# Kernel optimization log

Measured on AMD Instinct MI355X. Metric: run time of the kernel, lower is better.

The kernel has to match this reference:

```python
import jax, jax.numpy as jnp
import numpy as np

N = 50000
E = 800000
IN_C, HID, OUT_C, HEADS = 128, 64, 32, 2
NEG_SLOPE = 0.2


def _add_self_loops(edge_index, n):
    loop = jnp.arange(n, dtype=edge_index.dtype)
    return jnp.concatenate([edge_index, jnp.stack([loop, loop])], axis=1)


def gcn_conv(x, edge_index, W, b, n):
    ei = _add_self_loops(edge_index, n)
    src, dst = ei[0], ei[1]
    h = x @ W                                    # [N, out]
    deg = jax.ops.segment_sum(jnp.ones_like(dst, dtype=h.dtype), dst, num_segments=n)
    dinv = jnp.where(deg > 0, jax.lax.rsqrt(deg), 0.0)
    norm = dinv[src] * dinv[dst]                 # [E2]
    out = jax.ops.segment_sum(h[src] * norm[:, None], dst, num_segments=n)
    return out + b


def gat_conv(x, edge_index, W, att_src, att_dst, b, n, heads, out_dim, concat):
    ei = _add_self_loops(edge_index, n)
    src, dst = ei[0], ei[1]
    h = (x @ W).reshape(n, heads, out_dim)       # [N, H, C]
    a_s = jnp.sum(h * att_src, axis=-1)          # [N, H]
    a_d = jnp.sum(h * att_dst, axis=-1)          # [N, H]
    e = a_s[src] + a_d[dst]                      # [E2, H]
    e = jnp.where(e > 0, e, NEG_SLOPE * e)       # leaky_relu
    # edge softmax grouped by destination node
    m = jax.ops.segment_max(e, dst, num_segments=n)          # [N, H]
    ex = jnp.exp(e - m[dst])
    s = jax.ops.segment_sum(ex, dst, num_segments=n)          # [N, H]
    alpha = ex / s[dst]                          # [E2, H]
    out = jax.ops.segment_sum(h[src] * alpha[:, :, None], dst, num_segments=n)  # [N, H, C]
    if concat:
        out = out.reshape(n, heads * out_dim)
    else:
        out = out.mean(axis=1)
    return out + b


def setup_inputs() -> dict:
    key = jax.random.key(0)
    ks = jax.random.split(key, 16)
    x = jax.random.normal(ks[0], (N, IN_C), dtype=jnp.float32)
    edge_index = jax.random.randint(ks[1], (2, E), 0, N, dtype=jnp.int64)

    def glorot(k, shape):
        fan = shape[0] + shape[-1]
        return jax.random.normal(k, shape, dtype=jnp.float32) * np.sqrt(2.0 / fan)

    return {
        "x": x,
        "edge_index": edge_index,
        "W1": glorot(ks[2], (IN_C, HID)),
        "b1": jnp.zeros((HID,), jnp.float32),
        "W2": glorot(ks[3], (HID, HID)),
        "b2": jnp.zeros((HID,), jnp.float32),
        "Wg1": glorot(ks[4], (HID, HEADS * HID)),
        "as1": glorot(ks[5], (HEADS, HID)),
        "ad1": glorot(ks[6], (HEADS, HID)),
        "bg1": jnp.zeros((HEADS * HID,), jnp.float32),
        "Wg2": glorot(ks[7], (HEADS * HID, HEADS * OUT_C)),
        "as2": glorot(ks[8], (HEADS, OUT_C)),
        "ad2": glorot(ks[9], (HEADS, OUT_C)),
        "bg2": jnp.zeros((OUT_C,), jnp.float32),
    }


def reference(x, edge_index, W1, b1, W2, b2, Wg1, as1, ad1, bg1, Wg2, as2, ad2, bg2):
    n = x.shape[0]
    h = jax.nn.relu(gcn_conv(x, edge_index, W1, b1, n))
    h = jax.nn.relu(gcn_conv(h, edge_index, W2, b2, n))
    h = jax.nn.relu(gat_conv(h, edge_index, Wg1, as1, ad1, bg1, n, HEADS, HID, True))
    h = gat_conv(h, edge_index, Wg2, as2, ad2, bg2, n, HEADS, OUT_C, False)
    return jax.nn.log_softmax(h, axis=1)
```

## Files before the change

kernel.cpp:

```cpp
#include <hip/hip_runtime.h>

#define NN 50000
#define EE 800000
#define NEG 0.2f
#define CAP 64
#define NBC 98
#define BSH2 9
#define CAPB 16384
#define PCH 3125

typedef long long i64;
typedef unsigned int u32;
typedef unsigned short u16;
typedef __attribute__((ext_vector_type(8))) short bf16x8;
typedef __attribute__((ext_vector_type(4))) float f32x4;

static __device__ __forceinline__ u16 f2bf(float f) {
  u32 u = __float_as_uint(f);
  u += 0x7FFFu + ((u >> 16) & 1u);
  return (u16)(u >> 16);
}
static __device__ __forceinline__ float bflo(u32 v) { return __uint_as_float(v << 16); }
static __device__ __forceinline__ float bfhi(u32 v) { return __uint_as_float(v & 0xffff0000u); }
static __device__ __forceinline__ u32 pack2bf(float a, float b) {
  return (u32)f2bf(a) | ((u32)f2bf(b) << 16);
}
static __device__ __forceinline__ void fma8(float* acc, int4 v, float a) {
  acc[0] += bflo(v.x) * a; acc[1] += bfhi(v.x) * a;
  acc[2] += bflo(v.y) * a; acc[3] += bfhi(v.y) * a;
  acc[4] += bflo(v.z) * a; acc[5] += bfhi(v.z) * a;
  acc[6] += bflo(v.w) * a; acc[7] += bfhi(v.w) * a;
}

__global__ void k_probe(const void* ei, int* flag, int* gcnt) {
  __shared__ int sbad[4];
  int t = threadIdx.x;
  if (t < NBC) gcnt[t] = 0;
  const i64* p = (const i64*)ei;
  i64 v = p[t];
  int bad = (v < 0 || v >= NN) ? 1 : 0;
  unsigned long long b = __ballot(bad);
  if ((t & 63) == 0) sbad[t >> 6] = (b != 0ULL);
  __syncthreads();
  if (t == 0) *flag = !(sbad[0] | sbad[1] | sbad[2] | sbad[3]);
}

static __device__ __forceinline__ int edge_at(const void* ei, int is64, int idx) {
  return is64 ? (int)((const i64*)ei)[idx] : ((const int*)ei)[idx];
}

__global__ void k_part(const void* ei, const int* flag, int* gcnt, u32* buf) {
  __shared__ u32 lbuf[PCH];
  __shared__ int hist[128], offb[128], curb[128], gbase[128], sc[128];
  int t = threadIdx.x;
  int is64 = *flag;
  if (t < 128) { hist[t] = 0; curb[t] = 0; }
  __syncthreads();
  int lo = blockIdx.x * PCH;

  for (int e = lo + t; e < lo + PCH; e += 256)
    atomicAdd(&hist[edge_at(ei, is64, EE + e) >> BSH2], 1);
  __syncthreads();

  if (t < 128) sc[t] = hist[t];
  __syncthreads();
  for (int o = 1; o < 128; o <<= 1) {
    int v = (t >= o && t < 128) ? sc[t - o] : 0;
    __syncthreads();
    if (t < 128) sc[t] += v;
    __syncthreads();
  }
  if (t < 128) offb[t] = sc[t] - hist[t];
  __syncthreads();

  for (int e = lo + t; e < lo + PCH; e += 256) {
    int s = edge_at(ei, is64, e);
    int d = edge_at(ei, is64, EE + e);
    int b = d >> BSH2;
    u32 v = (u32)s | ((u32)(d & 511) << 16) | ((u32)b << 25);
    int p = atomicAdd(&curb[b], 1);
    lbuf[offb[b] + p] = v;
  }
  __syncthreads();

  if (t < 128) {
    int c = hist[t];
    gbase[t] = c ? atomicAdd(&gcnt[t], c) : 0;
  }
  __syncthreads();

  for (int i = t; i < PCH; i += 256) {
    u32 v = lbuf[i];
    int b = v >> 25;
    int pos = gbase[b] + (i - offb[b]);
    if (pos < CAPB) buf[(size_t)b * CAPB + pos] = v;
  }
}

__global__ void k_scanb(const int* gcnt, int* csrbase, int* rowp) {
  __shared__ int sc[128];
  int t = threadIdx.x;
  int c = (t < NBC) ? min(gcnt[t], CAPB) : 0;
  sc[t] = c;
  __syncthreads();
  for (int o = 1; o < 128; o <<= 1) {
    int v = (t >= o) ? sc[t - o] : 0;
    __syncthreads();
    sc[t] += v;
    __syncthreads();
  }
  if (t < NBC) csrbase[t] = sc[t] - c;
  if (t == 127) rowp[NN] = sc[127];
}

__global__ void k_csr2(const u32* __restrict__ buf, const int* __restrict__ gcnt,
                       const int* __restrict__ csrbase, int* __restrict__ rowp,
                       float* __restrict__ dinv, int* __restrict__ csr) {
  __shared__ int hist[512], offs[512], cur[512], sc[256];
  int b = blockIdx.x;
  int t = threadIdx.x;
  int cnt = min(gcnt[b], CAPB);
  const u32* mb = buf + (size_t)b * CAPB;
  int cbase = csrbase[b];
  int nbase = b << BSH2;
  int nn = min(512, NN - nbase);
  hist[t] = 0; hist[t + 256] = 0; cur[t] = 0; cur[t + 256] = 0;
  __syncthreads();
  for (int i = t; i < cnt; i += 256) atomicAdd(&hist[(mb[i] >> 16) & 511], 1);
  __syncthreads();
  int a0 = hist[2 * t], a1 = hist[2 * t + 1];
  sc[t] = a0 + a1;
  __syncthreads();
  for (int o = 1; o < 256; o <<= 1) {
    int v = (t >= o) ? sc[t - o] : 0;
    __syncthreads();
    sc[t] += v;
    __syncthreads();
  }
  int excl = sc[t] - (a0 + a1);
  offs[2 * t] = excl; offs[2 * t + 1] = excl + a0;
  __syncthreads();
  for (int i = t; i < nn; i += 256) {
    rowp[nbase + i] = cbase + offs[i];
    dinv[nbase + i] = rsqrtf((float)(hist[i] + 1));
  }
  for (int i = t; i < cnt; i += 256) {
    u32 v = mb[i];
    int dl = (v >> 16) & 511;
    int p = atomicAdd(&cur[dl], 1);
    csr[cbase + offs[dl] + p] = (int)(v & 0xFFFF);
  }
}

template <int K, int N, bool SRCF32, bool ATT, int NTH>
__global__ void k_mm(const void* __restrict__ Xsrc, const float* __restrict__ W,
                     const float* __restrict__ aw_s, const float* __restrict__ aw_d,
                     u16* __restrict__ Y, float* __restrict__ a_sv,
                     float* __restrict__ a_dv) {
  constexpr int BM = 64;
  constexpr int NT = N / 16;
  constexpr int KS = K / 32;
  __shared__ u16 Ab[BM * K];
  __shared__ u16 Wt[N * K];
  int t = threadIdx.x;
  int blockRow = blockIdx.x * BM;

  if (SRCF32) {
    const float4* Xq = (const float4*)Xsrc + (size_t)blockRow * (K / 4);
    for (int i = t; i < BM * K / 4; i += 256) {
      int r = (i * 4) / K;
      float4 v = (blockRow + r < NN) ? Xq[i] : make_float4(0.f, 0.f, 0.f, 0.f);
      ushort4 p = make_ushort4(f2bf(v.x), f2bf(v.y), f2bf(v.z), f2bf(v.w));
      int b = i * 8;
      *(ushort4*)((char*)Ab + (b ^ ((r & 7) << 4))) = p;
    }
  } else {
    const int4* Xq = (const int4*)Xsrc + (size_t)blockRow * (K / 8);
    for (int i = t; i < BM * K / 8; i += 256) {
      int r = (i * 8) / K;
      int4 v = (blockRow + r < NN) ? Xq[i] : make_int4(0, 0, 0, 0);
      int b = i * 16;
      *(int4*)((char*)Ab + (b ^ ((r & 7) << 4))) = v;
    }
  }
  for (int i = t; i < K * N; i += 256) {
    int k = i / N, n = i % N;
    int b = (n * K + k) * 2;
    *(u16*)((char*)Wt + (b ^ ((n & 7) << 4))) = f2bf(W[i]);
  }
  __syncthreads();

  int w = t >> 6, l = t & 63;
  int lr = l & 15, lg = l >> 4;
  int sw = (lr & 7) << 4;
  f32x4 acc[NT];
#pragma unroll
  for (int nt = 0; nt < NT; ++nt) acc[nt] = (f32x4)0.f;

#pragma unroll
  for (int ks = 0; ks < KS; ++ks) {
    int ar = 16 * w + lr;
    int ab = (ar * K + ks * 32 + lg * 8) * 2;
    bf16x8 af = *(bf16x8*)((char*)Ab + (ab ^ sw));
#pragma unroll
    for (int nt = 0; nt < NT; ++nt) {
      int bb = ((nt * 16 + lr) * K + ks * 32 + lg * 8) * 2;
      bf16x8 bfr = *(bf16x8*)((char*)Wt + (bb ^ sw));
      acc[nt] = __builtin_amdgcn_mfma_f32_16x16x32_bf16(af, bfr, acc[nt], 0, 0, 0);
    }
  }

#pragma unroll
  for (int j = 0; j < 4; ++j) {
    int row = blockRow + 16 * w + lg * 4 + j;
    if (row < NN) {
      u16* yr = Y + (size_t)row * N + lr;
#pragma unroll
      for (int nt = 0; nt < NT; ++nt) yr[nt * 16] = f2bf(acc[nt][j]);
    }
  }

  if (ATT) {
    float aws[NT], awd[NT];
#pragma unroll
    for (int nt = 0; nt < NT; ++nt) {
      aws[nt] = aw_s[nt * 16 + lr];
      awd[nt] = aw_d[nt * 16 + lr];
    }
#pragma unroll
    for (int j = 0; j < 4; ++j) {
      int row = blockRow + 16 * w + lg * 4 + j;
#pragma unroll
      for (int h = 0; h < 2; ++h) {
        float s = 0.f, d = 0.f;
#pragma unroll
        for (int q = 0; q < NTH; ++q) {
          int nt = h * NTH + q;
          s += acc[nt][j] * aws[nt];
          d += acc[nt][j] * awd[nt];
        }
#pragma unroll
        for (int mm = 8; mm >= 1; mm >>= 1) {
          s += __shfl_xor(s, mm, 64);
          d += __shfl_xor(d, mm, 64);
        }
        if (lr == 0 && row < NN) {
          a_sv[row * 2 + h] = s;
          a_dv[row * 2 + h] = d;
        }
      }
    }
  }
}

__global__ void k_gcn(const u16* __restrict__ g, const float* __restrict__ dinv,
                      const int* __restrict__ rowp, const int* __restrict__ csr,
                      const float* __restrict__ bias, u16* __restrict__ outb) {
  __shared__ int   s_src[16][CAP];
  __shared__ float s_wt[16][CAP];
  int w = (threadIdx.x >> 6) & 3;
  int lane = threadIdx.x & 63;
  int qd = lane >> 4, ql = lane & 15;
  int node = (blockIdx.x * 4 + w) * 4 + qd;
  int ns = w * 4 + qd;
  float di = dinv[node];
  int beg = rowp[node], cnt = rowp[node + 1] - beg;
  int tot = cnt + 1;
  int c1 = min(tot, CAP);
  int c1p = (c1 + 1) & ~1;

  for (int idx = ql; idx < c1p; idx += 16) {
    int s; float wt;
    if (idx < cnt)      { s = csr[beg + idx]; wt = dinv[s]; }
    else if (idx < tot) { s = node; wt = di; }
    else                { s = node; wt = 0.f; }
    s_src[ns][idx] = s; s_wt[ns][idx] = wt;
  }

  int sg = ql >> 3, q = ql & 7;
  const int4* g4 = (const int4*)g;
  float acc[8] = {0.f, 0.f, 0.f, 0.f, 0.f, 0.f, 0.f, 0.f};
  int nsteps = c1p >> 1;
  int s0 = s_src[ns][sg]; float a0 = s_wt[ns][sg];
  int4 v0 = g4[(size_t)s0 * 8 + q];
  for (int p = 1; p < nsteps; ++p) {
    int i1 = sg + 2 * p;
    int s1 = s_src[ns][i1]; float a1 = s_wt[ns][i1];
    int4 v1 = g4[(size_t)s1 * 8 + q];
    fma8(acc, v0, a0);
    v0 = v1; a0 = a1;
  }
  fma8(acc, v0, a0);
  for (int idx = CAP + sg; idx < tot; idx += 2) {
    int s = (idx < cnt) ? csr[beg + idx] : node;
    float a = (idx < cnt) ? dinv[s] : di;
    fma8(acc, g4[(size_t)s * 8 + q], a);
  }
#pragma unroll
  for (int j = 0; j < 8; ++j) acc[j] += __shfl_xor(acc[j], 8, 64);
  if (sg == 0) {
    u32 o[4];
#pragma unroll
    for (int p = 0; p < 4; ++p) {
      float v0f = fmaxf(acc[2 * p] * di + bias[8 * q + 2 * p], 0.f);
      float v1f = fmaxf(acc[2 * p + 1] * di + bias[8 * q + 2 * p + 1], 0.f);
      o[p] = pack2bf(v0f, v1f);
    }
    ((int4*)outb)[(size_t)node * 8 + q] = *(int4*)o;
  }
}

__global__ void k_gat1(const u16* __restrict__ hg, const float* __restrict__ a_s,
                       const float* __restrict__ a_d, const int* __restrict__ rowp,
                       const int* __restrict__ csr, const float* __restrict__ bias,
                       u16* __restrict__ outb) {
  __shared__ int   s_src[8][CAP];
  __shared__ float s_x[8][CAP][2];
  int w = (threadIdx.x >> 6) & 3;
  int lane = threadIdx.x & 63;
  int hf = lane >> 5, hl = lane & 31;
  int node = (blockIdx.x * 4 + w) * 2 + hf;
  int ns = w * 2 + hf;
  int beg = rowp[node], cnt = rowp[node + 1] - beg;
  int tot = cnt + 1;
  int c1 = min(tot, CAP);
  int c1p = (c1 + 1) & ~1;
  float ad0 = a_d[node * 2], ad1 = a_d[node * 2 + 1];

  float mm0 = -1e30f, mm1 = -1e30f;
  for (int idx = hl; idx < c1p; idx += 32) {
    int s = (idx < cnt) ? csr[beg + idx] : node;
    float e0 = -1e30f, e1 = -1e30f;
    if (idx < tot) {
      float2 av = ((const float2*)a_s)[s];
      e0 = av.x + ad0; e0 = e0 > 0.f ? e0 : NEG * e0;
      e1 = av.y + ad1; e1 = e1 > 0.f ? e1 : NEG * e1;
    }
    s_src[ns][idx] = s; s_x[ns][idx][0] = e0; s_x[ns][idx][1] = e1;
    mm0 = fmaxf(mm0, e0); mm1 = fmaxf(mm1, e1);
  }
  for (int idx = CAP + hl; idx < tot; idx += 32) {
    int s = (idx < cnt) ? csr[beg + idx] : node;
    float2 av = ((const float2*)a_s)[s];
    float e0 = av.x + ad0; e0 = e0 > 0.f ? e0 : NEG * e0;
    float e1 = av.y + ad1; e1 = e1 > 0.f ? e1 : NEG * e1;
    mm0 = fmaxf(mm0, e0); mm1 = fmaxf(mm1, e1);
  }
#pragma unroll
  for (int m = 16; m >= 1; m >>= 1) {
    mm0 = fmaxf(mm0, __shfl_xor(mm0, m, 64));
    mm1 = fmaxf(mm1, __shfl_xor(mm1, m, 64));
  }
  float ss0 = 0.f, ss1 = 0.f;
  for (int idx = hl; idx < c1p; idx += 32) {
    float x0 = __expf(s_x[ns][idx][0] - mm0), x1 = __expf(s_x[ns][idx][1] - mm1);
    s_x[ns][idx][0] = x0; s_x[ns][idx][1] = x1;
    ss0 += x0; ss1 += x1;
  }
  for (int idx = CAP + hl; idx < tot; idx += 32) {
    int s = (idx < cnt) ? csr[beg + idx] : node;
    float2 av = ((const float2*)a_s)[s];
    float e0 = av.x + ad0; e0 = e0 > 0.f ? e0 : NEG * e0;
    float e1 = av.y + ad1; e1 = e1 > 0.f ? e1 : NEG * e1;
    ss0 += __expf(e0 - mm0); ss1 += __expf(e1 - mm1);
  }
#pragma unroll
  for (int m = 16; m >= 1; m >>= 1) {
    ss0 += __shfl_xor(ss0, m, 64);
    ss1 += __shfl_xor(ss1, m, 64);
  }
  float inv0 = 1.f / ss0, inv1 = 1.f / ss1;

  int sg = hl >> 4, q = hl & 15;
  int hh = q >> 3;
  const int4* g4 = (const int4*)hg;
  float acc[8] = {0.f, 0.f, 0.f, 0.f, 0.f, 0.f, 0.f, 0.f};
  int nsteps = c1p >> 1;
  int s0 = s_src[ns][sg]; float a0 = s_x[ns][sg][hh];
  int4 v0 = g4[(size_t)s0 * 16 + q];
  for (int p = 1; p < nsteps; ++p) {
    int i1 = sg + 2 * p;
    int s1 = s_src[ns][i1]; float a1 = s_x[ns][i1][hh];
    int4 v1 = g4[(size_t)s1 * 16 + q];
    fma8(acc, v0, a0);
    v0 = v1; a0 = a1;
  }
  fma8(acc, v0, a0);
  for (int idx = CAP + sg; idx < tot; idx += 2) {
    int s = (idx < cnt) ? csr[beg + idx] : node;
    float e = (hh ? a_s[s * 2 + 1] + ad1 : a_s[s * 2] + ad0);
    e = e > 0.f ? e : NEG * e;
    float a = __expf(e - (hh ? mm1 : mm0));
    fma8(acc, g4[(size_t)s * 16 + q], a);
  }
#pragma unroll
  for (int j = 0; j < 8; ++j) acc[j] += __shfl_xor(acc[j], 16, 64);
  if (sg == 0) {
    float invh = hh ? inv1 : inv0;
    u32 o[4];
#pragma unroll
    for (int p = 0; p < 4; ++p) {
      float v0f = fmaxf(acc[2 * p] * invh + bias[8 * q + 2 * p], 0.f);
      float v1f = fmaxf(acc[2 * p + 1] * invh + bias[8 * q + 2 * p + 1], 0.f);
      o[p] = pack2bf(v0f, v1f);
    }
    ((int4*)outb)[(size_t)node * 16 + q] = *(int4*)o;
  }
}

__global__ void k_gat2(const u16* __restrict__ hg, const float* __restrict__ a_s,
                       const float* __restrict__ a_d, const int* __restrict__ rowp,
                       const int* __restrict__ csr, const float* __restrict__ bias,
                       float* __restrict__ out) {
  __shared__ int   s_src[16][CAP];
  __shared__ float s_x[16][CAP][2];
  int w = (threadIdx.x >> 6) & 3;
  int lane = threadIdx.x & 63;
  int qd = lane >> 4, ql = lane & 15;
  int node = (blockIdx.x * 4 + w) * 4 + qd;
  int ns = w * 4 + qd;
  int beg = rowp[node], cnt = rowp[node + 1] - beg;
  int tot = cnt + 1;
  int c1 = min(tot, CAP);
  int c1p = (c1 + 1) & ~1;
  float ad0 = a_d[node * 2], ad1 = a_d[node * 2 + 1];

  float mm0 = -1e30f, mm1 = -1e30f;
  for (int idx = ql; idx < c1p; idx += 16) {
    int s = (idx < cnt) ? csr[beg + idx] : node;
    float e0 = -1e30f, e1 = -1e30f;
    if (idx < tot) {
      float2 av = ((const float2*)a_s)[s];
      e0 = av.x + ad0; e0 = e0 > 0.f ? e0 : NEG * e0;
      e1 = av.y + ad1; e1 = e1 > 0.f ? e1 : NEG * e1;
    }
    s_src[ns][idx] = s; s_x[ns][idx][0] = e0; s_x[ns][idx][1] = e1;
    mm0 = fmaxf(mm0, e0); mm1 = fmaxf(mm1, e1);
  }
  for (int idx = CAP + ql; idx < tot; idx += 16) {
    int s = (idx < cnt) ? csr[beg + idx] : node;
    float2 av = ((const float2*)a_s)[s];
    float e0 = av.x + ad0; e0 = e0 > 0.f ? e0 : NEG * e0;
    float e1 = av.y + ad1; e1 = e1 > 0.f ? e1 : NEG * e1;
    mm0 = fmaxf(mm0, e0); mm1 = fmaxf(mm1, e1);
  }
#pragma unroll
  for (int m = 8; m >= 1; m >>= 1) {
    mm0 = fmaxf(mm0, __shfl_xor(mm0, m, 64));
    mm1 = fmaxf(mm1, __shfl_xor(mm1, m, 64));
  }
  float ss0 = 0.f, ss1 = 0.f;
  for (int idx = ql; idx < c1p; idx += 16) {
    float x0 = __expf(s_x[ns][idx][0] - mm0), x1 = __expf(s_x[ns][idx][1] - mm1);
    s_x[ns][idx][0] = x0; s_x[ns][idx][1] = x1;
    ss0 += x0; ss1 += x1;
  }
  for (int idx = CAP + ql; idx < tot; idx += 16) {
    int s = (idx < cnt) ? csr[beg + idx] : node;
    float2 av = ((const float2*)a_s)[s];
    float e0 = av.x + ad0; e0 = e0 > 0.f ? e0 : NEG * e0;
    float e1 = av.y + ad1; e1 = e1 > 0.f ? e1 : NEG * e1;
    ss0 += __expf(e0 - mm0); ss1 += __expf(e1 - mm1);
  }
#pragma unroll
  for (int m = 8; m >= 1; m >>= 1) {
    ss0 += __shfl_xor(ss0, m, 64);
    ss1 += __shfl_xor(ss1, m, 64);
  }
  float inv0 = 1.f / ss0, inv1 = 1.f / ss1;

  int sg = ql >> 3, q = ql & 7;
  int hh = q >> 2;
  const int4* g4 = (const int4*)hg;
  float acc[8] = {0.f, 0.f, 0.f, 0.f, 0.f, 0.f, 0.f, 0.f};
  int nsteps = c1p >> 1;
  int s0 = s_src[ns][sg]; float a0 = s_x[ns][sg][hh];
  int4 v0 = g4[(size_t)s0 * 8 + q];
  for (int p = 1; p < nsteps; ++p) {
    int i1 = sg + 2 * p;
    int s1 = s_src[ns][i1]; float a1 = s_x[ns][i1][hh];
    int4 v1 = g4[(size_t)s1 * 8 + q];
    fma8(acc, v0, a0);
    v0 = v1; a0 = a1;
  }
  fma8(acc, v0, a0);
  for (int idx = CAP + sg; idx < tot; idx += 2) {
    int s = (idx < cnt) ? csr[beg + idx] : node;
    float e = (hh ? a_s[s * 2 + 1] + ad1 : a_s[s * 2] + ad0);
    e = e > 0.f ? e : NEG * e;
    float a = __expf(e - (hh ? mm1 : mm0));
    fma8(acc, g4[(size_t)s * 8 + q], a);
  }
#pragma unroll
  for (int j = 0; j < 8; ++j) acc[j] += __shfl_xor(acc[j], 8, 64);

  float invh = hh ? inv1 : inv0;
  float vv[8];
#pragma unroll
  for (int j = 0; j < 8; ++j) {
    float a = acc[j] * invh;
    vv[j] = 0.5f * (a + __shfl_xor(a, 4, 64)) + bias[8 * (q & 3) + j];
  }
  float mx = vv[0];
#pragma unroll
  for (int j = 1; j < 8; ++j) mx = fmaxf(mx, vv[j]);
  mx = fmaxf(mx, __shfl_xor(mx, 1, 64));
  mx = fmaxf(mx, __shfl_xor(mx, 2, 64));
  float se = 0.f;
#pragma unroll
  for (int j = 0; j < 8; ++j) se += __expf(vv[j] - mx);
  se += __shfl_xor(se, 1, 64);
  se += __shfl_xor(se, 2, 64);
  float lse = mx + __logf(se);
  if (ql < 4) {
    float4 o0 = make_float4(vv[0] - lse, vv[1] - lse, vv[2] - lse, vv[3] - lse);
    float4 o1 = make_float4(vv[4] - lse, vv[5] - lse, vv[6] - lse, vv[7] - lse);
    float4* orow = (float4*)(out + (size_t)node * 32);
    orow[q * 2] = o0;
    orow[q * 2 + 1] = o1;
  }
}

extern "C" void kernel_launch(void* const* d_in, const int* in_sizes, int n_in,
                              void* d_out, int out_size, void* d_ws, size_t ws_size,
                              hipStream_t stream) {
  (void)in_sizes; (void)n_in; (void)out_size; (void)ws_size;
  const float* x   = (const float*)d_in[0];
  const void*  ei  = d_in[1];
  const float* W1  = (const float*)d_in[2];
  const float* b1  = (const float*)d_in[3];
  const float* W2  = (const float*)d_in[4];
  const float* b2  = (const float*)d_in[5];
  const float* Wg1 = (const float*)d_in[6];
  const float* as1 = (const float*)d_in[7];
  const float* ad1 = (const float*)d_in[8];
  const float* bg1 = (const float*)d_in[9];
  const float* Wg2 = (const float*)d_in[10];
  const float* as2 = (const float*)d_in[11];
  const float* ad2 = (const float*)d_in[12];
  const float* bg2 = (const float*)d_in[13];
  float* out = (float*)d_out;

  char* w = (char*)d_ws;
  auto alloc = [&](size_t bytes) { char* p = w; w += (bytes + 255) & ~(size_t)255; return p; };
  u16* Hb     = (u16*)alloc((size_t)NN * 128 * 2);
  u16* Xb     = (u16*)alloc((size_t)NN * 128 * 2);
  float* dinv = (float*)alloc((size_t)NN * 4);
  float* asb  = (float*)alloc((size_t)NN * 2 * 4);
  float* adb  = (float*)alloc((size_t)NN * 2 * 4);
  int* rowp   = (int*)alloc((size_t)(NN + 1) * 4);
  int* csr    = (int*)alloc((size_t)EE * 4);
  u32* buf    = (u32*)alloc((size_t)NBC * CAPB * 4);
  int* gcnt   = (int*)alloc((size_t)NBC * 4);
  int* csrbase= (int*)alloc((size_t)NBC * 4);
  int* flag   = (int*)alloc(16);

  const int TB = 256;
  int gQ = 3125;
  int gH = 6250;
  int gG = (NN + 63) / 64;

  k_probe<<<1, 256, 0, stream>>>(ei, flag, gcnt);
  k_part<<<256, TB, 0, stream>>>(ei, flag, gcnt, buf);
  k_scanb<<<1, 128, 0, stream>>>(gcnt, csrbase, rowp);
  k_csr2<<<NBC, TB, 0, stream>>>(buf, gcnt, csrbase, rowp, dinv, csr);

  k_mm<128, 64, true, false, 0><<<gG, TB, 0, stream>>>(x, W1, nullptr, nullptr, Hb, nullptr, nullptr);
  k_gcn<<<gQ, TB, 0, stream>>>(Hb, dinv, rowp, csr, b1, Xb);
  k_mm<64, 64, false, false, 0><<<gG, TB, 0, stream>>>(Xb, W2, nullptr, nullptr, Hb, nullptr, nullptr);
  k_gcn<<<gQ, TB, 0, stream>>>(Hb, dinv, rowp, csr, b2, Xb);
  k_mm<64, 128, false, true, 4><<<gG, TB, 0, stream>>>(Xb, Wg1, as1, ad1, Hb, asb, adb);
  k_gat1<<<gH, TB, 0, stream>>>(Hb, asb, adb, rowp, csr, bg1, Xb);
  k_mm<128, 64, false, true, 2><<<gG, TB, 0, stream>>>(Xb, Wg2, as2, ad2, Hb, asb, adb);
  k_gat2<<<gQ, TB, 0, stream>>>(Hb, asb, adb, rowp, csr, bg2, out);
}
```

Baseline: 190.4 us.

## Prepack weights once and fold probe and scan kernels into neighbors

Weights are converted to bf16 and swizzled once in a small prep kernel, so each GEMM block copies the packed tile with vector loads instead of converting per block. The probe kernel is folded into k_part: every block redoes the int64 check on its first 256 entries. The bucket scan is folded into k_csr2, where each block recomputes the 98-entry prefix sum. This cuts launches and repeated weight conversion at the cost of some redundant per-block work and a memset.

```diff
diff --git a/kernel.cpp b/kernel.cpp
--- a/kernel.cpp
+++ b/kernel.cpp
@@ -32,30 +32,38 @@
   acc[6] += bflo(v.w) * a; acc[7] += bfhi(v.w) * a;
 }
 
-__global__ void k_probe(const void* ei, int* flag, int* gcnt) {
-  __shared__ int sbad[4];
-  int t = threadIdx.x;
-  if (t < NBC) gcnt[t] = 0;
-  const i64* p = (const i64*)ei;
-  i64 v = p[t];
-  int bad = (v < 0 || v >= NN) ? 1 : 0;
-  unsigned long long b = __ballot(bad);
-  if ((t & 63) == 0) sbad[t >> 6] = (b != 0ULL);
-  __syncthreads();
-  if (t == 0) *flag = !(sbad[0] | sbad[1] | sbad[2] | sbad[3]);
-}
-
 static __device__ __forceinline__ int edge_at(const void* ei, int is64, int idx) {
   return is64 ? (int)((const i64*)ei)[idx] : ((const int*)ei)[idx];
 }
 
-__global__ void k_part(const void* ei, const int* flag, int* gcnt, u32* buf) {
+__global__ void k_prep(const float* __restrict__ W1, const float* __restrict__ W2,
+                       const float* __restrict__ Wg1, const float* __restrict__ Wg2,
+                       u16* P1, u16* P2, u16* P3, u16* P4) {
+  int b = blockIdx.x, t = threadIdx.x;
+  const float* W; u16* P; int K, N;
+  if (b == 0)      { W = W1;  P = P1; K = 128; N = 64;  }
+  else if (b == 1) { W = W2;  P = P2; K = 64;  N = 64;  }
+  else if (b == 2) { W = Wg1; P = P3; K = 64;  N = 128; }
+  else             { W = Wg2; P = P4; K = 128; N = 64;  }
+  for (int i = t; i < K * N; i += 256) {
+    int k = i / N, n = i % N;
+    int byte = ((n * K + k) * 2) ^ ((n & 7) << 4);
+    *(u16*)((char*)P + byte) = f2bf(W[i]);
+  }
+}
+
+__global__ void k_part(const void* ei, int* gcnt, u32* buf) {
   __shared__ u32 lbuf[PCH];
-  __shared__ int hist[128], offb[128], curb[128], gbase[128], sc[128];
+  __shared__ int hist[128], offb[128], curb[128], gbase[128], sc[128], sb[4];
   int t = threadIdx.x;
-  int is64 = *flag;
+  const i64* p64 = (const i64*)ei;
+  i64 pv = p64[t];
+  int bad = (pv < 0 || pv >= NN) ? 1 : 0;
+  unsigned long long bm = __ballot(bad);
+  if ((t & 63) == 0) sb[t >> 6] = (bm != 0ULL);
   if (t < 128) { hist[t] = 0; curb[t] = 0; }
   __syncthreads();
+  int is64 = !(sb[0] | sb[1] | sb[2] | sb[3]);
   int lo = blockIdx.x * PCH;
 
   for (int e = lo + t; e < lo + PCH; e += 256)
@@ -97,35 +105,30 @@
   }
 }
 
-__global__ void k_scanb(const int* gcnt, int* csrbase, int* rowp) {
-  __shared__ int sc[128];
-  int t = threadIdx.x;
-  int c = (t < NBC) ? min(gcnt[t], CAPB) : 0;
-  sc[t] = c;
-  __syncthreads();
-  for (int o = 1; o < 128; o <<= 1) {
-    int v = (t >= o) ? sc[t - o] : 0;
-    __syncthreads();
-    sc[t] += v;
-    __syncthreads();
-  }
-  if (t < NBC) csrbase[t] = sc[t] - c;
-  if (t == 127) rowp[NN] = sc[127];
-}
-
 __global__ void k_csr2(const u32* __restrict__ buf, const int* __restrict__ gcnt,
-                       const int* __restrict__ csrbase, int* __restrict__ rowp,
-                       float* __restrict__ dinv, int* __restrict__ csr) {
-  __shared__ int hist[512], offs[512], cur[512], sc[256];
+                       int* __restrict__ rowp, float* __restrict__ dinv,
+                       int* __restrict__ csr) {
+  __shared__ int hist[512], offs[512], cur[512], sc[256], pscan[128];
   int b = blockIdx.x;
   int t = threadIdx.x;
   int cnt = min(gcnt[b], CAPB);
   const u32* mb = buf + (size_t)b * CAPB;
-  int cbase = csrbase[b];
   int nbase = b << BSH2;
   int nn = min(512, NN - nbase);
+
+  int pc = (t < NBC) ? min(gcnt[t], CAPB) : 0;
+  if (t < 128) pscan[t] = pc;
   hist[t] = 0; hist[t + 256] = 0; cur[t] = 0; cur[t + 256] = 0;
   __syncthreads();
+  for (int o = 1; o < 128; o <<= 1) {
+    int v = (t >= o && t < 128) ? pscan[t - o] : 0;
+    __syncthreads();
+    if (t < 128) pscan[t] += v;
+    __syncthreads();
+  }
+  int cbase = pscan[b] - cnt;
+  if (b == NBC - 1 && t == 0) rowp[NN] = pscan[NBC - 1];
+
   for (int i = t; i < cnt; i += 256) atomicAdd(&hist[(mb[i] >> 16) & 511], 1);
   __syncthreads();
   int a0 = hist[2 * t], a1 = hist[2 * t + 1];
@@ -153,7 +156,7 @@
 }
 
 template <int K, int N, bool SRCF32, bool ATT, int NTH>
-__global__ void k_mm(const void* __restrict__ Xsrc, const float* __restrict__ W,
+__global__ void k_mm(const void* __restrict__ Xsrc, const u16* __restrict__ Wp,
                      const float* __restrict__ aw_s, const float* __restrict__ aw_d,
                      u16* __restrict__ Y, float* __restrict__ a_sv,
                      float* __restrict__ a_dv) {
@@ -183,11 +186,8 @@
       *(int4*)((char*)Ab + (b ^ ((r & 7) << 4))) = v;
     }
   }
-  for (int i = t; i < K * N; i += 256) {
-    int k = i / N, n = i % N;
-    int b = (n * K + k) * 2;
-    *(u16*)((char*)Wt + (b ^ ((n & 7) << 4))) = f2bf(W[i]);
-  }
+  for (int i = t; i < N * K / 8; i += 256)
+    ((int4*)Wt)[i] = ((const int4*)Wp)[i];
   __syncthreads();
 
   int w = t >> 6, l = t & 63;
@@ -552,25 +552,27 @@
   int* csr    = (int*)alloc((size_t)EE * 4);
   u32* buf    = (u32*)alloc((size_t)NBC * CAPB * 4);
   int* gcnt   = (int*)alloc((size_t)NBC * 4);
-  int* csrbase= (int*)alloc((size_t)NBC * 4);
-  int* flag   = (int*)alloc(16);
+  u16* Wp1    = (u16*)alloc(128 * 64 * 2);
+  u16* Wp2    = (u16*)alloc(64 * 64 * 2);
+  u16* Wp3    = (u16*)alloc(64 * 128 * 2);
+  u16* Wp4    = (u16*)alloc(128 * 64 * 2);
 
   const int TB = 256;
   int gQ = 3125;
   int gH = 6250;
   int gG = (NN + 63) / 64;
 
-  k_probe<<<1, 256, 0, stream>>>(ei, flag, gcnt);
-  k_part<<<256, TB, 0, stream>>>(ei, flag, gcnt, buf);
-  k_scanb<<<1, 128, 0, stream>>>(gcnt, csrbase, rowp);
-  k_csr2<<<NBC, TB, 0, stream>>>(buf, gcnt, csrbase, rowp, dinv, csr);
-
-  k_mm<128, 64, true, false, 0><<<gG, TB, 0, stream>>>(x, W1, nullptr, nullptr, Hb, nullptr, nullptr);
+  hipMemsetAsync(gcnt, 0, (size_t)NBC * 4, stream);
+  k_prep<<<4, 256, 0, stream>>>(W1, W2, Wg1, Wg2, Wp1, Wp2, Wp3, Wp4);
+  k_part<<<256, TB, 0, stream>>>(ei, gcnt, buf);
+  k_csr2<<<NBC, TB, 0, stream>>>(buf, gcnt, rowp, dinv, csr);
+
+  k_mm<128, 64, true, false, 0><<<gG, TB, 0, stream>>>(x, Wp1, nullptr, nullptr, Hb, nullptr, nullptr);
   k_gcn<<<gQ, TB, 0, stream>>>(Hb, dinv, rowp, csr, b1, Xb);
-  k_mm<64, 64, false, false, 0><<<gG, TB, 0, stream>>>(Xb, W2, nullptr, nullptr, Hb, nullptr, nullptr);
+  k_mm<64, 64, false, false, 0><<<gG, TB, 0, stream>>>(Xb, Wp2, nullptr, nullptr, Hb, nullptr, nullptr);
   k_gcn<<<gQ, TB, 0, stream>>>(Hb, dinv, rowp, csr, b2, Xb);
-  k_mm<64, 128, false, true, 4><<<gG, TB, 0, stream>>>(Xb, Wg1, as1, ad1, Hb, asb, adb);
+  k_mm<64, 128, false, true, 4><<<gG, TB, 0, stream>>>(Xb, Wp3, as1, ad1, Hb, asb, adb);
   k_gat1<<<gH, TB, 0, stream>>>(Hb, asb, adb, rowp, csr, bg1, Xb);
-  k_mm<128, 64, false, true, 2><<<gG, TB, 0, stream>>>(Xb, Wg2, as2, ad2, Hb, asb, adb);
+  k_mm<128, 64, false, true, 2><<<gG, TB, 0, stream>>>(Xb, Wp4, as2, ad2, Hb, asb, adb);
   k_gat2<<<gQ, TB, 0, stream>>>(Hb, asb, adb, rowp, csr, bg2, out);
 }
```

Measured after the change: 191.5 us. Within noise of the previous version (+0.6%).
